# Performance work log

Hardware: AMD Instinct MI355X
Metric: run time of the kernel (lower is better)

The kernel has to match this reference:

```python
import jax, jax.numpy as jnp
import numpy as np

B, T, C, H, W = 2, 20, 128, 128, 128
D_MODEL = 256
N_HEAD = 16
D_K = 4
MLP_OUT = 128
PE_T = 1000.0
EPS = 1e-5


def setup_inputs() -> dict:
    key = jax.random.key(0)
    ks = jax.random.split(key, 16)
    x = jax.random.normal(ks[0], (B, T, C, H, W), jnp.float32)
    batch_positions = jnp.sort(
        jax.random.randint(ks[1], (B, T), 0, 365).astype(jnp.int32), axis=1)
    qk_std = float(np.sqrt(2.0 / D_K))
    return {
        "x": x,
        "batch_positions": batch_positions,
        # GroupNorm(n_head, in_channels)
        "in_norm_w": jnp.ones((C,), jnp.float32),
        "in_norm_b": jnp.zeros((C,), jnp.float32),
        # Conv1d(in_channels, d_model, 1) -> weight (d_model, in_channels)
        "inconv_w": jax.random.normal(ks[2], (D_MODEL, C), jnp.float32) / np.sqrt(C),
        "inconv_b": jax.random.normal(ks[3], (D_MODEL,), jnp.float32) * 0.01,
        # learnable query (n_head, d_k), std sqrt(2/d_k)
        "Q": jax.random.normal(ks[4], (N_HEAD, D_K), jnp.float32) * qk_std,
        # fc1_k: Linear(d_model, n_head*d_k)
        "k_w": jax.random.normal(ks[5], (N_HEAD * D_K, D_MODEL), jnp.float32) * qk_std,
        "k_b": jax.random.normal(ks[6], (N_HEAD * D_K,), jnp.float32) * 0.01,
        # MLP: Linear(256, 128) + LayerNorm(128)
        "mlp_w": jax.random.normal(ks[7], (MLP_OUT, D_MODEL), jnp.float32) / np.sqrt(D_MODEL),
        "mlp_b": jax.random.normal(ks[8], (MLP_OUT,), jnp.float32) * 0.01,
        "ln_w": jnp.ones((MLP_OUT,), jnp.float32),
        "ln_b": jnp.zeros((MLP_OUT,), jnp.float32),
        # out GroupNorm(n_head, mlp[-1])
        "out_norm_w": jnp.ones((MLP_OUT,), jnp.float32),
        "out_norm_b": jnp.zeros((MLP_OUT,), jnp.float32),
    }


def _ltae_forward(x, batch_positions, in_norm_w, in_norm_b, inconv_w, inconv_b,
                  Q, k_w, k_b, mlp_w, mlp_b, ln_w, ln_b, out_norm_w, out_norm_b):
    b, t, c, h, w = x.shape
    n_head, d_k = Q.shape
    n = b * h * w
    # (B,T,C,H,W) -> (N, T, C), N = B*H*W ordered (b, h, w)
    out = jnp.transpose(x, (0, 3, 4, 1, 2)).reshape(n, t, c)

    # in_norm: GroupNorm(groups=n_head) over (group-channels, T) per sample
    cg = c // n_head
    xg = out.reshape(n, t, n_head, cg)
    mu = xg.mean(axis=(1, 3), keepdims=True)
    var = xg.var(axis=(1, 3), keepdims=True)
    out = ((xg - mu) / jnp.sqrt(var + EPS)).reshape(n, t, c) * in_norm_w + in_norm_b

    # inconv: 1x1 Conv1d == per-timestep linear (C -> d_model)
    out = out @ inconv_w.T + inconv_b  # (N, T, d_model)
    d_model = out.shape[-1]

    # sinusoidal positional encoding (d_model//n_head dims, repeated n_head times)
    d_pe = d_model // n_head
    i = jnp.arange(d_pe)
    denom = PE_T ** (2.0 * (i // 2).astype(out.dtype) / d_pe)
    bp = batch_positions.astype(out.dtype)  # (B, T)
    tab = bp[:, :, None] / denom            # (B, T, d_pe)
    pe = jnp.where(i % 2 == 0, jnp.sin(tab), jnp.cos(tab))
    pe = jnp.tile(pe, (1, 1, n_head))        # (B, T, d_model)
    out = (out.reshape(b, h, w, t, d_model) + pe[:, None, None]).reshape(n, t, d_model)

    # multi-head attention pooling with one learnable query per head
    k = (out @ k_w.T + k_b).reshape(n, t, n_head, d_k)
    scores = jnp.einsum('nthd,hd->nht', k, Q) / jnp.sqrt(jnp.asarray(d_k, out.dtype))
    attn = jax.nn.softmax(scores, axis=-1)             # (N, H, T)
    vh = out.reshape(n, t, n_head, d_model // n_head)  # head h = channel slice
    pooled = jnp.einsum('nht,nthe->nhe', attn, vh).reshape(n, d_model)

    # MLP: Linear -> LayerNorm -> GELU (exact)
    h1 = pooled @ mlp_w.T + mlp_b
    mu = h1.mean(-1, keepdims=True)
    var = h1.var(-1, keepdims=True)
    h1 = (h1 - mu) / jnp.sqrt(var + EPS) * ln_w + ln_b
    h1 = jax.nn.gelu(h1, approximate=False)

    # out_norm: GroupNorm(n_head) on (N, mlp_out) -> stats over each group's channels
    co = h1.shape[-1]
    xg = h1.reshape(n, n_head, co // n_head)
    mu = xg.mean(-1, keepdims=True)
    var = xg.var(-1, keepdims=True)
    h1 = ((xg - mu) / jnp.sqrt(var + EPS)).reshape(n, co) * out_norm_w + out_norm_b

    return h1.reshape(b, h, w, co).transpose(0, 3, 1, 2)  # (B, mlp_out, H, W)


def reference(x, batch_positions, in_norm_w, in_norm_b, inconv_w, inconv_b,
              Q, k_w, k_b, mlp_w, mlp_b, ln_w, ln_b, out_norm_w, out_norm_b):
    return _ltae_forward(x, batch_positions, in_norm_w, in_norm_b, inconv_w,
                         inconv_b, Q, k_w, k_b, mlp_w, mlp_b, ln_w, ln_b,
                         out_norm_w, out_norm_b)
```

## Files before the change

### kernel.cpp

```cpp
#include <hip/hip_runtime.h>
#include <hip/hip_fp16.h>

typedef _Float16 h2  __attribute__((ext_vector_type(2)));
typedef _Float16 v8h __attribute__((ext_vector_type(8)));
typedef float    f4  __attribute__((ext_vector_type(4)));
typedef uint4 u128;

#define T_    20
#define C_    128
#define HW_   16384
#define NH_   16
#define TILE_ 16
#define EPSV  1e-5f

#define OFF_SW   0
#define OFF_SC   4096
#define OFF_WC   8192
#define OFF_MW   73728
#define OFF_PBT  139264
#define OFF_MB2  141312

__device__ __forceinline__ float fdot2f(h2 a, h2 b, float c) {
#if __has_builtin(__builtin_amdgcn_fdot2)
  return __builtin_amdgcn_fdot2(a, b, c, false);
#else
  return c + (float)a[0]*(float)b[0] + (float)a[1]*(float)b[1];
#endif
}

__device__ __forceinline__ v8h zero8() {
  v8h r;
  #pragma unroll
  for (int i = 0; i < 8; ++i) r[i] = (_Float16)0.f;
  return r;
}

__global__ void __launch_bounds__(256) ltae_prep(
    const int* __restrict__ bp, const float* __restrict__ gw, const float* __restrict__ gb,
    const float* __restrict__ icw, const float* __restrict__ icb,
    const float* __restrict__ Qm, const float* __restrict__ kw, const float* __restrict__ kb,
    const float* __restrict__ mw, const float* __restrict__ mb,
    unsigned char* __restrict__ ws)
{
  const int tid = threadIdx.x;
  const int blk = blockIdx.x;
  _Float16* SWh = (_Float16*)(ws + OFF_SW);
  float*    SC  = (float*)(ws + OFF_SC);
  _Float16* WCf = (_Float16*)(ws + OFF_WC);
  _Float16* MWf = (_Float16*)(ws + OFF_MW);
  _Float16* PBT = (_Float16*)(ws + OFF_PBT);
  float*    MB2 = (float*)(ws + OFF_MB2);

  __shared__ float qwl[16*256];
  __shared__ float bcl[256];
  __shared__ float pet[2*20*16];
  __shared__ float qbl[16];
  __shared__ float qwsl[16*16];

  if (blk < 4) {
    for (int o = tid; o < 512; o += 256) {
      int h = 4*blk + (o >> 7), c = o & 127;
      float q0 = Qm[h*4+0], q1 = Qm[h*4+1], q2 = Qm[h*4+2], q3 = Qm[h*4+3];
      const float* k0 = kw + (4*h+0)*256;
      const float* k1 = kw + (4*h+1)*256;
      const float* k2 = kw + (4*h+2)*256;
      const float* k3 = kw + (4*h+3)*256;
      float acc = 0.f;
      for (int d = 0; d < 256; ++d) {
        float qwd = k0[d]*q0 + k1[d]*q1 + k2[d]*q2 + k3[d]*q3;
        acc = fmaf(icw[d*128 + c], qwd, acc);
      }
      SWh[h*128 + c] = (_Float16)(acc * gw[c]);
    }
  } else if (blk < 6) {
    int base = (blk - 4) * 16384;
    for (int o = tid; o < 16384; o += 256) {
      int idx = base + o;
      WCf[idx] = (_Float16)(icw[idx] * gw[idx & 127]);
    }
  } else if (blk < 8) {
    int base = (blk - 6) * 16384;
    for (int o = tid; o < 16384; o += 256)
      MWf[base + o] = (_Float16)mw[base + o];
  } else if (blk == 8) {
    if (tid < 256) {
      float a = icb[tid];
      for (int c2 = 0; c2 < 128; ++c2) a = fmaf(gb[c2], icw[tid*128 + c2], a);
      bcl[tid] = a;
    }
    __syncthreads();
    if (tid < 128) {
      float a = mb[tid];
      for (int d = 0; d < 256; ++d) a = fmaf(bcl[d], mw[tid*256 + d], a);
      MB2[tid] = a;
    }
  } else {
    for (int o = tid; o < 4096; o += 256) {
      int h = o >> 8, d = o & 255;
      qwl[o] = kw[(4*h+0)*256+d]*Qm[h*4+0] + kw[(4*h+1)*256+d]*Qm[h*4+1]
             + kw[(4*h+2)*256+d]*Qm[h*4+2] + kw[(4*h+3)*256+d]*Qm[h*4+3];
    }
    if (tid < 256) {
      float a = icb[tid];
      for (int c2 = 0; c2 < 128; ++c2) a = fmaf(gb[c2], icw[tid*128 + c2], a);
      bcl[tid] = a;
    }
    for (int o = tid; o < 640; o += 256) {
      int bb = o / 320, rem = o % 320;
      int t = rem >> 4, e = rem & 15;
      float pos = (float)bp[bb*T_ + t];
      float den = powf(1000.f, (float)(2*(e>>1)) / 16.f);
      float v = pos / den;
      pet[o] = (e & 1) ? cosf(v) : sinf(v);
    }
    __syncthreads();
    if (tid < 16) {
      qbl[tid] = kb[tid*4+0]*Qm[tid*4+0] + kb[tid*4+1]*Qm[tid*4+1]
               + kb[tid*4+2]*Qm[tid*4+2] + kb[tid*4+3]*Qm[tid*4+3];
    }
    if (tid < 256) {
      int h = tid >> 4, e = tid & 15;
      float a = 0.f;
      for (int m2 = 0; m2 < 16; ++m2) a += qwl[h*256 + m2*16 + e];
      qwsl[tid] = a;
    }
    __syncthreads();
    for (int o = tid; o < 640; o += 256) {
      int bb = o / 320, rem = o % 320;
      int t = rem >> 4, h = rem & 15;
      float a = qbl[h];
      for (int d = 0; d < 256; ++d) a = fmaf(bcl[d], qwl[h*256 + d], a);
      for (int e = 0; e < 16; ++e) a = fmaf(pet[(bb*T_ + t)*16 + e], qwsl[h*16 + e], a);
      SC[(bb*T_ + t)*NH_ + h] = 0.5f * a;
    }
    for (int o = tid; o < 1024; o += 256) {
      int bb = o >> 9, e = (o >> 5) & 15, tp = o & 31;
      PBT[o] = (tp < T_) ? (_Float16)pet[(bb*T_ + tp)*16 + e] : (_Float16)0.f;
    }
  }
}

__global__ void __launch_bounds__(256, 2) ltae_main(
    const float* __restrict__ x, const unsigned char* __restrict__ ws,
    float* __restrict__ out,
    const float* __restrict__ lnw, const float* __restrict__ lnb,
    const float* __restrict__ onw, const float* __restrict__ onb)
{
  __shared__ __align__(16) unsigned char lds[81920];
  const int tid = threadIdx.x;
  const int s = tid >> 4, q = tid & 15;
  const int lane = tid & 63;

  int bid = (int)blockIdx.x;
  int L = (bid & 7) * 256 + (bid >> 3);
  const int n0 = L * TILE_;
  const int b  = n0 >> 14;
  const int r0 = n0 & 16383;

  #define XS(row, chunk) ((unsigned char*)lds + (row)*256 + ((((chunk) ^ ((row)&7))) << 4))

  float gsum = 0.f, gsq = 0.f;
  {
    const float* p = x + (size_t)b*(T_*C_*HW_) + (size_t)(q*8)*HW_ + r0 + s;
    for (int t = 0; t < T_; ++t) {
      float v[8];
      #pragma unroll
      for (int i = 0; i < 8; ++i) v[i] = p[(size_t)i*HW_];
      p += (size_t)C_*HW_;
      #pragma unroll
      for (int i = 0; i < 8; ++i) { gsum += v[i]; gsq = fmaf(v[i], v[i], gsq); }
      u128 pk; h2* ph = (h2*)&pk;
      #pragma unroll
      for (int i = 0; i < 4; ++i) { h2 t2; t2[0] = (_Float16)v[2*i]; t2[1] = (_Float16)v[2*i+1]; ph[i] = t2; }
      *(u128*)XS(t*16 + s, q) = pk;
    }
  }
  float mug[16], invg[16];
  {
    float mu  = gsum * (1.f/160.f);
    float var = fmaf(-mu, mu, gsq * (1.f/160.f));
    float inv = rsqrtf(var + EPSV);
    int lb = lane & 48;
    #pragma unroll
    for (int g = 0; g < 16; ++g) {
      mug[g]  = __shfl(mu,  lb + g, 64);
      invg[g] = __shfl(inv, lb + g, 64);
    }
  }
  __syncthreads();

  float a_[T_];
  {
    h2 sw[64];
    {
      const u128* sp = (const u128*)(ws + OFF_SW) + q*16;
      #pragma unroll
      for (int i = 0; i < 16; ++i) ((u128*)sw)[i] = sp[i];
    }
    float K0 = 0.f;
    #pragma unroll
    for (int g = 0; g < 16; ++g) {
      float ss = 0.f;
      #pragma unroll
      for (int k = 0; k < 4; ++k) ss += (float)sw[g*4+k][0] + (float)sw[g*4+k][1];
      K0 = fmaf(invg[g]*mug[g], ss, K0);
    }
    const float* SCp = (const float*)(ws + OFF_SC) + (b*T_)*NH_ + q;
    #pragma unroll
    for (int t = 0; t < T_; ++t) {
      int row = t*16 + s;
      float accE = 0.f, accO = 0.f;
      #pragma unroll
      for (int g = 0; g < 16; g += 2) {
        u128 u0 = *(const u128*)XS(row, g);
        u128 u1 = *(const u128*)XS(row, g+1);
        h2* x0 = (h2*)&u0; h2* x1 = (h2*)&u1;
        float s0 = 0.f, s1 = 0.f;
        #pragma unroll
        for (int k = 0; k < 4; ++k) {
          s0 = fdot2f(x0[k], sw[g*4+k],     s0);
          s1 = fdot2f(x1[k], sw[(g+1)*4+k], s1);
        }
        accE = fmaf(invg[g],   s0, accE);
        accO = fmaf(invg[g+1], s1, accO);
      }
      a_[t] = 0.5f*((accE + accO) - K0) + SCp[t*NH_];
    }
  }
  h2 ah[T_];
  {
    float m = a_[0];
    #pragma unroll
    for (int t = 1; t < T_; ++t) m = fmaxf(m, a_[t]);
    float Z = 0.f;
    #pragma unroll
    for (int t = 0; t < T_; ++t) { a_[t] = __expf(a_[t] - m); Z += a_[t]; }
    float rZ = 1.f / Z;
    #pragma unroll
    for (int t = 0; t < T_; ++t) {
      a_[t] *= rZ;
      _Float16 af = (_Float16)a_[t];
      h2 t2; t2[0] = af; t2[1] = af; ah[t] = t2;
    }
  }

  #pragma unroll 1
  for (int g = 0; g < 16; ++g) {
    h2 accA[4], accB[4];
    #pragma unroll
    for (int k = 0; k < 4; ++k) { accA[k][0]=(_Float16)0.f; accA[k][1]=(_Float16)0.f;
                                  accB[k][0]=(_Float16)0.f; accB[k][1]=(_Float16)0.f; }
    #pragma unroll
    for (int t = 0; t < T_; t += 2) {
      u128 u0 = *(const u128*)XS(t*16 + s, g);
      u128 u1 = *(const u128*)XS((t+1)*16 + s, g);
      h2* x0 = (h2*)&u0; h2* x1 = (h2*)&u1;
      #pragma unroll
      for (int k = 0; k < 4; ++k) {
        accA[k] = ah[t]  * x0[k] + accA[k];
        accB[k] = ah[t+1]* x1[k] + accB[k];
      }
    }
    __syncthreads();
    u128 pk; h2* ph = (h2*)&pk;
    #pragma unroll
    for (int k = 0; k < 4; ++k) {
      float lo = (float)accA[k][0] + (float)accB[k][0];
      float hi = (float)accA[k][1] + (float)accB[k][1];
      lo = invg[g]*(lo - mug[g]);
      hi = invg[g]*(hi - mug[g]);
      h2 t2; t2[0] = (_Float16)lo; t2[1] = (_Float16)hi; ph[k] = t2;
    }
    *(u128*)XS(q*16 + s, g) = pk;
  }

  {
    unsigned char* atl = lds + 65536 + (q*16 + s)*48;
    u128 pk0, pk1, pk2;
    h2* p0 = (h2*)&pk0; h2* p1 = (h2*)&pk1; h2* p2 = (h2*)&pk2;
    #pragma unroll
    for (int k = 0; k < 4; ++k) { h2 t2; t2[0]=(_Float16)a_[2*k];   t2[1]=(_Float16)a_[2*k+1]; p0[k]=t2; }
    #pragma unroll
    for (int k = 0; k < 4; ++k) { h2 t2; t2[0]=(_Float16)a_[8+2*k]; t2[1]=(_Float16)a_[9+2*k]; p1[k]=t2; }
    #pragma unroll
    for (int k = 0; k < 4; ++k) {
      h2 t2;
      t2[0] = (k<2) ? (_Float16)a_[16+2*k] : (_Float16)0.f;
      t2[1] = (k<2) ? (_Float16)a_[17+2*k] : (_Float16)0.f;
      p2[k]=t2;
    }
    *(u128*)(atl) = pk0; *(u128*)(atl+16) = pk1; *(u128*)(atl+32) = pk2;
  }
  __syncthreads();

  const int wid = tid >> 6;
  const int lr = lane & 15, lk = lane >> 4;
  f4 pacc[4];
  {
    const _Float16* WC  = (const _Float16*)(ws + OFF_WC);
    const _Float16* PBT = (const _Float16*)(ws + OFF_PBT);
    #pragma unroll
    for (int hh = 0; hh < 4; ++hh) {
      int h = wid*4 + hh;
      f4 acc = {0.f,0.f,0.f,0.f};
      #pragma unroll
      for (int ks = 0; ks < 4; ++ks) {
        v8h A = *(const v8h*)XS(h*16 + lr, ks*4 + lk);
        v8h B = *(const v8h*)(WC + (16*h + lr)*128 + ks*32 + lk*8);
        acc = __builtin_amdgcn_mfma_f32_16x16x32_f16(A, B, acc, 0, 0, 0);
      }
      {
        v8h A = zero8();
        if (lk < 3) A = *(const v8h*)(lds + 65536 + (h*16 + lr)*48 + lk*16);
        v8h B = *(const v8h*)(PBT + (b*16 + lr)*32 + lk*8);
        acc = __builtin_amdgcn_mfma_f32_16x16x32_f16(A, B, acc, 0, 0, 0);
      }
      pacc[hh] = acc;
    }
  }
  __syncthreads();
  #pragma unroll
  for (int hh = 0; hh < 4; ++hh) {
    int d = 16*(wid*4 + hh) + lr;
    #pragma unroll
    for (int r = 0; r < 4; ++r) {
      int sp = 4*lk + r;
      *(_Float16*)(lds + ((sp*512 + d*2) ^ ((sp&7)<<4))) = (_Float16)pacc[hh][r];
    }
  }
  __syncthreads();

  f4 m0 = {0.f,0.f,0.f,0.f}, m1 = {0.f,0.f,0.f,0.f};
  {
    const _Float16* MW = (const _Float16*)(ws + OFF_MW);
    #pragma unroll
    for (int ks = 0; ks < 8; ++ks) {
      int d0 = ks*32 + lk*8;
      v8h A  = *(const v8h*)(lds + ((lr*512 + d0*2) ^ ((lr&7)<<4)));
      v8h B0 = *(const v8h*)(MW + (32*wid + lr)*256 + d0);
      v8h B1 = *(const v8h*)(MW + (32*wid + 16 + lr)*256 + d0);
      m0 = __builtin_amdgcn_mfma_f32_16x16x32_f16(A, B0, m0, 0,0,0);
      m1 = __builtin_amdgcn_mfma_f32_16x16x32_f16(A, B1, m1, 0,0,0);
    }
  }
  {
    const float* MB2 = (const float*)(ws + OFF_MB2);
    int j0 = 32*wid + lr, j1 = 32*wid + 16 + lr;
    float b0 = MB2[j0], b1 = MB2[j1];
    #pragma unroll
    for (int r = 0; r < 4; ++r) {
      int sp = 4*lk + r;
      *(float*)(lds + 8192 + ((sp*512 + j0*4) ^ ((sp&7)<<4))) = m0[r] + b0;
      *(float*)(lds + 8192 + ((sp*512 + j1*4) ^ ((sp&7)<<4))) = m1[r] + b1;
    }
  }
  __syncthreads();

  {
    float4 A0 = *(const float4*)(lds + 8192 + (((s*512 + q*32)      ) ^ ((s&7)<<4)));
    float4 A1 = *(const float4*)(lds + 8192 + (((s*512 + q*32 + 16) ) ^ ((s&7)<<4)));
    float h1v[8] = {A0.x,A0.y,A0.z,A0.w,A1.x,A1.y,A1.z,A1.w};
    float sum = 0.f, sq = 0.f;
    #pragma unroll
    for (int i = 0; i < 8; ++i) { sum += h1v[i]; sq = fmaf(h1v[i], h1v[i], sq); }
    #pragma unroll
    for (int d = 1; d < 16; d <<= 1) { sum += __shfl_xor(sum, d, 64); sq += __shfl_xor(sq, d, 64); }
    float mu1 = sum * (1.f/128.f);
    float vr1 = fmaf(-mu1, mu1, sq * (1.f/128.f));
    float is1 = rsqrtf(vr1 + EPSV);
    float4 lwa = *(const float4*)(lnw + 8*q), lwb = *(const float4*)(lnw + 8*q + 4);
    float4 lba = *(const float4*)(lnb + 8*q), lbb = *(const float4*)(lnb + 8*q + 4);
    float lw[8] = {lwa.x,lwa.y,lwa.z,lwa.w,lwb.x,lwb.y,lwb.z,lwb.w};
    float lb2[8] = {lba.x,lba.y,lba.z,lba.w,lbb.x,lbb.y,lbb.z,lbb.w};
    float yv[8]; float s2 = 0.f, q2 = 0.f;
    #pragma unroll
    for (int i = 0; i < 8; ++i) {
      float g_ = (h1v[i]-mu1)*is1*lw[i] + lb2[i];
      float y  = 0.5f*g_*(1.f + erff(g_*0.70710678118654752f));
      yv[i] = y; s2 += y; q2 = fmaf(y, y, q2);
    }
    s2 *= 0.125f;
    float v2 = fmaf(-s2, s2, q2*0.125f);
    float iv2 = rsqrtf(v2 + EPSV);
    float4 owa = *(const float4*)(onw + 8*q), owb = *(const float4*)(onw + 8*q + 4);
    float4 oba = *(const float4*)(onb + 8*q), obb = *(const float4*)(onb + 8*q + 4);
    float ow[8] = {owa.x,owa.y,owa.z,owa.w,owb.x,owb.y,owb.z,owb.w};
    float ob[8] = {oba.x,oba.y,oba.z,oba.w,obb.x,obb.y,obb.z,obb.w};
    float* op = out + (size_t)(b*128 + 8*q)*HW_ + r0 + s;
    #pragma unroll
    for (int i = 0; i < 8; ++i)
      op[(size_t)i*HW_] = (yv[i]-s2)*iv2*ow[i] + ob[i];
  }
  #undef XS
}

extern "C" void kernel_launch(void* const* d_in, const int* in_sizes, int n_in,
                              void* d_out, int out_size, void* d_ws, size_t ws_size,
                              hipStream_t stream) {
  const float* x   = (const float*)d_in[0];
  const int*   bp  = (const int*)d_in[1];
  const float* gw  = (const float*)d_in[2];
  const float* gb  = (const float*)d_in[3];
  const float* icw = (const float*)d_in[4];
  const float* icb = (const float*)d_in[5];
  const float* Qm  = (const float*)d_in[6];
  const float* kw  = (const float*)d_in[7];
  const float* kb  = (const float*)d_in[8];
  const float* mw  = (const float*)d_in[9];
  const float* mb  = (const float*)d_in[10];
  const float* lnw = (const float*)d_in[11];
  const float* lnb = (const float*)d_in[12];
  const float* onw = (const float*)d_in[13];
  const float* onb = (const float*)d_in[14];
  unsigned char* ws = (unsigned char*)d_ws;

  hipLaunchKernelGGL(ltae_prep, dim3(10), dim3(256), 0, stream,
                     bp, gw, gb, icw, icb, Qm, kw, kb, mw, mb, ws);
  hipLaunchKernelGGL(ltae_main, dim3(2048), dim3(256), 0, stream,
                     x, ws, (float*)d_out, lnw, lnb, onw, onb);
}
```

Baseline: 657.4 us.

## Restructure main kernel for 512 threads with MFMA attention scores and vectorized I/O

The main kernel moves to 512-thread blocks. Input loads become float4 reads across pixels, GroupNorm statistics are reduced through LDS, and the input is normalized before it is stored. Attention scores are computed with MFMA instead of fdot2 loops, and the weighted pooling is remapped across threads using shuffles. The output is transposed through LDS so stores are float4. The prep kernel splits the SW computation over 16 blocks. Together these aim to cut global memory transactions, raise occupancy and shorten the prep kernel, at the cost of more barriers, more shuffle traffic and higher register pressure.

After: 603.3 us. 8.2% less time.

```diff
diff --git a/kernel.cpp b/kernel.cpp
--- a/kernel.cpp
+++ b/kernel.cpp
@@ -20,20 +20,14 @@
 #define OFF_PBT  139264
 #define OFF_MB2  141312
 
-__device__ __forceinline__ float fdot2f(h2 a, h2 b, float c) {
-#if __has_builtin(__builtin_amdgcn_fdot2)
-  return __builtin_amdgcn_fdot2(a, b, c, false);
-#else
-  return c + (float)a[0]*(float)b[0] + (float)a[1]*(float)b[1];
-#endif
-}
-
 __device__ __forceinline__ v8h zero8() {
   v8h r;
   #pragma unroll
   for (int i = 0; i < 8; ++i) r[i] = (_Float16)0.f;
   return r;
 }
+__device__ __forceinline__ int h2i(h2 v) { union { h2 h; int i; } u; u.h = v; return u.i; }
+__device__ __forceinline__ h2  ih2(int v) { union { h2 h; int i; } u; u.i = v; return u.h; }
 
 __global__ void __launch_bounds__(256) ltae_prep(
     const int* __restrict__ bp, const float* __restrict__ gw, const float* __restrict__ gb,
@@ -56,33 +50,36 @@
   __shared__ float pet[2*20*16];
   __shared__ float qbl[16];
   __shared__ float qwsl[16*16];
-
-  if (blk < 4) {
-    for (int o = tid; o < 512; o += 256) {
-      int h = 4*blk + (o >> 7), c = o & 127;
-      float q0 = Qm[h*4+0], q1 = Qm[h*4+1], q2 = Qm[h*4+2], q3 = Qm[h*4+3];
-      const float* k0 = kw + (4*h+0)*256;
-      const float* k1 = kw + (4*h+1)*256;
-      const float* k2 = kw + (4*h+2)*256;
-      const float* k3 = kw + (4*h+3)*256;
-      float acc = 0.f;
-      for (int d = 0; d < 256; ++d) {
-        float qwd = k0[d]*q0 + k1[d]*q1 + k2[d]*q2 + k3[d]*q3;
-        acc = fmaf(icw[d*128 + c], qwd, acc);
-      }
-      SWh[h*128 + c] = (_Float16)(acc * gw[c]);
-    }
-  } else if (blk < 6) {
-    int base = (blk - 4) * 16384;
+  __shared__ float red[256];
+
+  if (blk < 16) {
+    int h = blk, dh = tid >> 7;
+    float q0 = Qm[h*4+0], q1 = Qm[h*4+1], q2 = Qm[h*4+2], q3 = Qm[h*4+3];
+    const float* k0 = kw + (4*h+0)*256;
+    const float* k1 = kw + (4*h+1)*256;
+    const float* k2 = kw + (4*h+2)*256;
+    const float* k3 = kw + (4*h+3)*256;
+    int c = tid & 127;
+    float acc = 0.f;
+    for (int d = 0; d < 128; ++d) {
+      int dg = dh*128 + d;
+      float qwd = k0[dg]*q0 + k1[dg]*q1 + k2[dg]*q2 + k3[dg]*q3;
+      acc = fmaf(icw[dg*128 + c], qwd, acc);
+    }
+    red[tid] = acc;
+    __syncthreads();
+    if (tid < 128) SWh[h*128 + tid] = (_Float16)((red[tid] + red[tid+128]) * gw[tid] * 0.5f);
+  } else if (blk < 18) {
+    int base = (blk - 16) * 16384;
     for (int o = tid; o < 16384; o += 256) {
       int idx = base + o;
       WCf[idx] = (_Float16)(icw[idx] * gw[idx & 127]);
     }
-  } else if (blk < 8) {
-    int base = (blk - 6) * 16384;
+  } else if (blk < 20) {
+    int base = (blk - 18) * 16384;
     for (int o = tid; o < 16384; o += 256)
       MWf[base + o] = (_Float16)mw[base + o];
-  } else if (blk == 8) {
+  } else if (blk == 20) {
     if (tid < 256) {
       float a = icb[tid];
       for (int c2 = 0; c2 < 128; ++c2) a = fmaf(gb[c2], icw[tid*128 + c2], a);
@@ -140,16 +137,17 @@
   }
 }
 
-__global__ void __launch_bounds__(256, 2) ltae_main(
+__global__ void __launch_bounds__(512, 4) ltae_main(
     const float* __restrict__ x, const unsigned char* __restrict__ ws,
     float* __restrict__ out,
     const float* __restrict__ lnw, const float* __restrict__ lnb,
     const float* __restrict__ onw, const float* __restrict__ onb)
 {
   __shared__ __align__(16) unsigned char lds[81920];
-  const int tid = threadIdx.x;
-  const int s = tid >> 4, q = tid & 15;
+  const int tid  = threadIdx.x;
   const int lane = tid & 63;
+  const int w    = tid >> 6;
+  const int m16  = lane & 15, kg = lane >> 4;
 
   int bid = (int)blockIdx.x;
   int L = (bid & 7) * 256 + (bid >> 3);
@@ -157,241 +155,325 @@
   const int b  = n0 >> 14;
   const int r0 = n0 & 16383;
 
-  #define XS(row, chunk) ((unsigned char*)lds + (row)*256 + ((((chunk) ^ ((row)&7))) << 4))
-
-  float gsum = 0.f, gsq = 0.f;
-  {
-    const float* p = x + (size_t)b*(T_*C_*HW_) + (size_t)(q*8)*HW_ + r0 + s;
-    for (int t = 0; t < T_; ++t) {
-      float v[8];
-      #pragma unroll
-      for (int i = 0; i < 8; ++i) v[i] = p[(size_t)i*HW_];
-      p += (size_t)C_*HW_;
-      #pragma unroll
-      for (int i = 0; i < 8; ++i) { gsum += v[i]; gsq = fmaf(v[i], v[i], gsq); }
-      u128 pk; h2* ph = (h2*)&pk;
-      #pragma unroll
-      for (int i = 0; i < 4; ++i) { h2 t2; t2[0] = (_Float16)v[2*i]; t2[1] = (_Float16)v[2*i+1]; ph[i] = t2; }
-      *(u128*)XS(t*16 + s, q) = pk;
-    }
-  }
-  float mug[16], invg[16];
-  {
-    float mu  = gsum * (1.f/160.f);
-    float var = fmaf(-mu, mu, gsq * (1.f/160.f));
-    float inv = rsqrtf(var + EPSV);
-    int lb = lane & 48;
-    #pragma unroll
-    for (int g = 0; g < 16; ++g) {
-      mug[g]  = __shfl(mu,  lb + g, 64);
-      invg[g] = __shfl(inv, lb + g, 64);
-    }
-  }
-  __syncthreads();
-
-  float a_[T_];
-  {
-    h2 sw[64];
-    {
-      const u128* sp = (const u128*)(ws + OFF_SW) + q*16;
-      #pragma unroll
-      for (int i = 0; i < 16; ++i) ((u128*)sw)[i] = sp[i];
-    }
-    float K0 = 0.f;
-    #pragma unroll
-    for (int g = 0; g < 16; ++g) {
-      float ss = 0.f;
-      #pragma unroll
-      for (int k = 0; k < 4; ++k) ss += (float)sw[g*4+k][0] + (float)sw[g*4+k][1];
-      K0 = fmaf(invg[g]*mug[g], ss, K0);
-    }
-    const float* SCp = (const float*)(ws + OFF_SC) + (b*T_)*NH_ + q;
-    #pragma unroll
-    for (int t = 0; t < T_; ++t) {
-      int row = t*16 + s;
-      float accE = 0.f, accO = 0.f;
-      #pragma unroll
-      for (int g = 0; g < 16; g += 2) {
-        u128 u0 = *(const u128*)XS(row, g);
-        u128 u1 = *(const u128*)XS(row, g+1);
-        h2* x0 = (h2*)&u0; h2* x1 = (h2*)&u1;
-        float s0 = 0.f, s1 = 0.f;
+#define XS(row, chunk) ((unsigned char*)lds + (row)*256 + \
+    ((((chunk) ^ (((row) ^ ((row) >> 4)) & 15))) << 4))
+#define PL(s, byteo) ((unsigned char*)lds + (s)*512 + \
+    (((((byteo) >> 4) ^ (((s)*2) & 31))) << 4) + ((byteo) & 15))
+#define HL(s, byteo) ((unsigned char*)lds + 8192 + (s)*512 + \
+    (((((byteo) >> 4) ^ (((s)*2) & 31))) << 4) + ((byteo) & 15))
+
+  {
+    const int sub = tid & 3, g = (tid >> 2) & 15, w8 = w;
+    uint2 hp[20];
+    float ps0=0,ps1=0,ps2=0,ps3=0, pq0=0,pq1=0,pq2=0,pq3=0;
+    const float* xb = x + (size_t)b*(T_*C_*HW_) + r0 + 4*sub;
+    #pragma unroll
+    for (int k = 0; k < 20; ++k) {
+      int j = w8 + 8*k;
+      int t = j >> 3, cg = j & 7, c = g*8 + cg;
+      float4 v = *(const float4*)(xb + (size_t)(t*C_ + c) * HW_);
+      ps0 += v.x; pq0 = fmaf(v.x, v.x, pq0);
+      ps1 += v.y; pq1 = fmaf(v.y, v.y, pq1);
+      ps2 += v.z; pq2 = fmaf(v.z, v.z, pq2);
+      ps3 += v.w; pq3 = fmaf(v.w, v.w, pq3);
+      h2 lo; lo[0] = (_Float16)v.x; lo[1] = (_Float16)v.y;
+      h2 hi; hi[0] = (_Float16)v.z; hi[1] = (_Float16)v.w;
+      hp[k] = make_uint2((unsigned)h2i(lo), (unsigned)h2i(hi));
+    }
+    unsigned char* scr = (unsigned char*)lds + 65536;
+    float psum[4] = {ps0,ps1,ps2,ps3}, psq[4] = {pq0,pq1,pq2,pq3};
+    #pragma unroll
+    for (int i = 0; i < 4; ++i) {
+      int s = 4*sub + i;
+      int word = w8*512 + g*32 + (((s + g) & 15) << 1);
+      *(float2*)(scr + word*4) = make_float2(psum[i], psq[i]);
+    }
+    __syncthreads();
+    float mu[4], inv[4];
+    #pragma unroll
+    for (int i = 0; i < 4; ++i) {
+      int s = 4*sub + i;
+      float su = 0.f, sq = 0.f;
+      #pragma unroll
+      for (int ww = 0; ww < 8; ++ww) {
+        float2 p = *(const float2*)(scr + (ww*512 + g*32 + (((s + g) & 15) << 1))*4);
+        su += p.x; sq += p.y;
+      }
+      float m_ = su * (1.f/160.f);
+      mu[i]  = m_;
+      inv[i] = rsqrtf(fmaf(-m_, m_, sq * (1.f/160.f)) + EPSV);
+    }
+#define P1WRITE(k) { \
+      int j = w8 + 8*(k); \
+      int t = j >> 3, cg = j & 7; \
+      h2 lo = ih2((int)hp[k].x), hi = ih2((int)hp[k].y); \
+      float f0 = ((float)lo[0] - mu[0]) * inv[0]; \
+      float f1 = ((float)lo[1] - mu[1]) * inv[1]; \
+      float f2 = ((float)hi[0] - mu[2]) * inv[2]; \
+      float f3 = ((float)hi[1] - mu[3]) * inv[3]; \
+      *(_Float16*)(XS(t*16 + 4*sub + 0, g) + cg*2) = (_Float16)f0; \
+      *(_Float16*)(XS(t*16 + 4*sub + 1, g) + cg*2) = (_Float16)f1; \
+      *(_Float16*)(XS(t*16 + 4*sub + 2, g) + cg*2) = (_Float16)f2; \
+      *(_Float16*)(XS(t*16 + 4*sub + 3, g) + cg*2) = (_Float16)f3; }
+    #pragma unroll
+    for (int k = 0; k < 16; ++k) P1WRITE(k)
+    __syncthreads();
+    #pragma unroll
+    for (int k = 16; k < 20; ++k) P1WRITE(k)
+#undef P1WRITE
+  }
+  __syncthreads();
+
+  float attA[2][4], attB[2][4];
+  {
+    v8h Bsw[4];
+    const _Float16* SWp = (const _Float16*)(ws + OFF_SW) + m16*128 + kg*8;
+    #pragma unroll
+    for (int ks = 0; ks < 4; ++ks) Bsw[ks] = *(const v8h*)(SWp + ks*32);
+    const float* SCb = (const float*)(ws + OFF_SC) + b*T_*NH_;
+    #pragma unroll
+    for (int si = 0; si < 2; ++si) {
+      int s = 2*w + si;
+      f4 a0 = {0.f,0.f,0.f,0.f}, a1 = {0.f,0.f,0.f,0.f};
+      #pragma unroll
+      for (int ks = 0; ks < 4; ++ks) {
+        v8h A = *(const v8h*)XS(m16*16 + s, ks*4 + kg);
+        a0 = __builtin_amdgcn_mfma_f32_16x16x32_f16(A, Bsw[ks], a0, 0, 0, 0);
+        v8h At = zero8();
+        if (m16 < 4) At = *(const v8h*)XS((16 + m16)*16 + s, ks*4 + kg);
+        a1 = __builtin_amdgcn_mfma_f32_16x16x32_f16(At, Bsw[ks], a1, 0, 0, 0);
+      }
+      float aa[4], ab[4] = {0.f,0.f,0.f,0.f};
+      #pragma unroll
+      for (int r = 0; r < 4; ++r) aa[r] = a0[r] + SCb[(4*kg + r)*NH_ + m16];
+      if (kg == 0) {
         #pragma unroll
-        for (int k = 0; k < 4; ++k) {
-          s0 = fdot2f(x0[k], sw[g*4+k],     s0);
-          s1 = fdot2f(x1[k], sw[(g+1)*4+k], s1);
-        }
-        accE = fmaf(invg[g],   s0, accE);
-        accO = fmaf(invg[g+1], s1, accO);
-      }
-      a_[t] = 0.5f*((accE + accO) - K0) + SCp[t*NH_];
-    }
-  }
-  h2 ah[T_];
-  {
-    float m = a_[0];
-    #pragma unroll
-    for (int t = 1; t < T_; ++t) m = fmaxf(m, a_[t]);
-    float Z = 0.f;
-    #pragma unroll
-    for (int t = 0; t < T_; ++t) { a_[t] = __expf(a_[t] - m); Z += a_[t]; }
-    float rZ = 1.f / Z;
-    #pragma unroll
-    for (int t = 0; t < T_; ++t) {
-      a_[t] *= rZ;
-      _Float16 af = (_Float16)a_[t];
-      h2 t2; t2[0] = af; t2[1] = af; ah[t] = t2;
-    }
-  }
-
-  #pragma unroll 1
-  for (int g = 0; g < 16; ++g) {
-    h2 accA[4], accB[4];
-    #pragma unroll
-    for (int k = 0; k < 4; ++k) { accA[k][0]=(_Float16)0.f; accA[k][1]=(_Float16)0.f;
-                                  accB[k][0]=(_Float16)0.f; accB[k][1]=(_Float16)0.f; }
-    #pragma unroll
-    for (int t = 0; t < T_; t += 2) {
-      u128 u0 = *(const u128*)XS(t*16 + s, g);
-      u128 u1 = *(const u128*)XS((t+1)*16 + s, g);
-      h2* x0 = (h2*)&u0; h2* x1 = (h2*)&u1;
-      #pragma unroll
-      for (int k = 0; k < 4; ++k) {
-        accA[k] = ah[t]  * x0[k] + accA[k];
-        accB[k] = ah[t+1]* x1[k] + accB[k];
-      }
-    }
-    __syncthreads();
-    u128 pk; h2* ph = (h2*)&pk;
-    #pragma unroll
-    for (int k = 0; k < 4; ++k) {
-      float lo = (float)accA[k][0] + (float)accB[k][0];
-      float hi = (float)accA[k][1] + (float)accB[k][1];
-      lo = invg[g]*(lo - mug[g]);
-      hi = invg[g]*(hi - mug[g]);
-      h2 t2; t2[0] = (_Float16)lo; t2[1] = (_Float16)hi; ph[k] = t2;
-    }
-    *(u128*)XS(q*16 + s, g) = pk;
-  }
-
-  {
-    unsigned char* atl = lds + 65536 + (q*16 + s)*48;
-    u128 pk0, pk1, pk2;
-    h2* p0 = (h2*)&pk0; h2* p1 = (h2*)&pk1; h2* p2 = (h2*)&pk2;
-    #pragma unroll
-    for (int k = 0; k < 4; ++k) { h2 t2; t2[0]=(_Float16)a_[2*k];   t2[1]=(_Float16)a_[2*k+1]; p0[k]=t2; }
-    #pragma unroll
-    for (int k = 0; k < 4; ++k) { h2 t2; t2[0]=(_Float16)a_[8+2*k]; t2[1]=(_Float16)a_[9+2*k]; p1[k]=t2; }
-    #pragma unroll
-    for (int k = 0; k < 4; ++k) {
-      h2 t2;
-      t2[0] = (k<2) ? (_Float16)a_[16+2*k] : (_Float16)0.f;
-      t2[1] = (k<2) ? (_Float16)a_[17+2*k] : (_Float16)0.f;
-      p2[k]=t2;
-    }
-    *(u128*)(atl) = pk0; *(u128*)(atl+16) = pk1; *(u128*)(atl+32) = pk2;
-  }
-  __syncthreads();
-
-  const int wid = tid >> 6;
-  const int lr = lane & 15, lk = lane >> 4;
-  f4 pacc[4];
+        for (int r = 0; r < 4; ++r) ab[r] = a1[r] + SCb[(16 + r)*NH_ + m16];
+      }
+      float mx = fmaxf(fmaxf(aa[0], aa[1]), fmaxf(aa[2], aa[3]));
+      if (kg == 0) mx = fmaxf(mx, fmaxf(fmaxf(ab[0], ab[1]), fmaxf(ab[2], ab[3])));
+      mx = fmaxf(mx, __shfl_xor(mx, 16, 64));
+      mx = fmaxf(mx, __shfl_xor(mx, 32, 64));
+      float Z = 0.f;
+      #pragma unroll
+      for (int r = 0; r < 4; ++r) { aa[r] = __expf(aa[r] - mx); Z += aa[r]; }
+      if (kg == 0) {
+        #pragma unroll
+        for (int r = 0; r < 4; ++r) { ab[r] = __expf(ab[r] - mx); Z += ab[r]; }
+      }
+      Z += __shfl_xor(Z, 16, 64);
+      Z += __shfl_xor(Z, 32, 64);
+      float rZ = 1.f / Z;
+      #pragma unroll
+      for (int r = 0; r < 4; ++r) {
+        attA[si][r] = aa[r] * rZ;
+        attB[si][r] = (kg == 0) ? ab[r] * rZ : 0.f;
+      }
+    }
+  }
+  int qi0,qi1,qi2,qi3, qb0,qb1,qb2,qb3;
+  {
+    h2 p;
+    p[0]=(_Float16)attA[0][0]; p[1]=(_Float16)attA[1][0]; qi0=h2i(p);
+    p[0]=(_Float16)attA[0][1]; p[1]=(_Float16)attA[1][1]; qi1=h2i(p);
+    p[0]=(_Float16)attA[0][2]; p[1]=(_Float16)attA[1][2]; qi2=h2i(p);
+    p[0]=(_Float16)attA[0][3]; p[1]=(_Float16)attA[1][3]; qi3=h2i(p);
+    p[0]=(_Float16)attB[0][0]; p[1]=(_Float16)attB[1][0]; qb0=h2i(p);
+    p[0]=(_Float16)attB[0][1]; p[1]=(_Float16)attB[1][1]; qb1=h2i(p);
+    p[0]=(_Float16)attB[0][2]; p[1]=(_Float16)attB[1][2]; qb2=h2i(p);
+    p[0]=(_Float16)attB[0][3]; p[1]=(_Float16)attB[1][3]; qb3=h2i(p);
+  }
+
+  const int sP = tid >> 5;
+  const int ll = lane & 31, hq = ll >> 3, cp = ll & 7;
+  const int hiHalf = (lane >> 5) & 1;
+  h2 acc0[4][8], acc1[4][8];
+  #pragma unroll
+  for (int i = 0; i < 4; ++i)
+    #pragma unroll
+    for (int c2 = 0; c2 < 8; ++c2) {
+      acc0[i][c2][0] = (_Float16)0.f; acc0[i][c2][1] = (_Float16)0.f;
+      acc1[i][c2][0] = (_Float16)0.f; acc1[i][c2][1] = (_Float16)0.f;
+    }
+  #pragma unroll
+  for (int t = 0; t < T_; t += 2) {
+    u128 u0 = *(const u128*)XS(t*16 + sP, 2*cp);
+    u128 u1 = *(const u128*)XS(t*16 + sP, 2*cp + 1);
+    u128 w0 = *(const u128*)XS((t+1)*16 + sP, 2*cp);
+    u128 w1 = *(const u128*)XS((t+1)*16 + sP, 2*cp + 1);
+    const h2* e0 = (const h2*)&u0; const h2* e1 = (const h2*)&u1;
+    const h2* f0 = (const h2*)&w0; const h2* f1 = (const h2*)&w1;
+    int qselE = (t < 16) ? (((t & 3) == 0) ? qi0 : qi2) : (((t & 3) == 0) ? qb0 : qb2);
+    int qselO = (t < 16) ? (((t & 3) == 0) ? qi1 : qi3) : (((t & 3) == 0) ? qb1 : qb3);
+    #pragma unroll
+    for (int i = 0; i < 4; ++i) {
+      int h = 4*hq + i;
+      int src = (t < 16) ? (h + ((t >> 2) << 4)) : h;
+      h2 pvE = ih2(__shfl(qselE, src, 64));
+      h2 pvO = ih2(__shfl(qselO, src, 64));
+      _Float16 aE = hiHalf ? pvE[1] : pvE[0];
+      _Float16 aO = hiHalf ? pvO[1] : pvO[0];
+      h2 aE2; aE2[0] = aE; aE2[1] = aE;
+      h2 aO2; aO2[0] = aO; aO2[1] = aO;
+      #pragma unroll
+      for (int c2 = 0; c2 < 4; ++c2) {
+        acc0[i][c2]     = aE2 * e0[c2] + acc0[i][c2];
+        acc0[i][4 + c2] = aE2 * e1[c2] + acc0[i][4 + c2];
+        acc1[i][c2]     = aO2 * f0[c2] + acc1[i][c2];
+        acc1[i][4 + c2] = aO2 * f1[c2] + acc1[i][4 + c2];
+      }
+    }
+  }
+  __syncthreads();
+  #pragma unroll
+  for (int i = 0; i < 4; ++i) {
+    int h = 4*hq + i;
+    u128 o0, o1;
+    h2* p0 = (h2*)&o0; h2* p1 = (h2*)&o1;
+    #pragma unroll
+    for (int c2 = 0; c2 < 8; ++c2) {
+      float lo = (float)acc0[i][c2][0] + (float)acc1[i][c2][0];
+      float hi = (float)acc0[i][c2][1] + (float)acc1[i][c2][1];
+      h2 t2; t2[0] = (_Float16)lo; t2[1] = (_Float16)hi;
+      if (c2 < 4) p0[c2] = t2; else p1[c2 - 4] = t2;
+    }
+    *(u128*)XS(h*16 + sP, 2*cp)     = o0;
+    *(u128*)XS(h*16 + sP, 2*cp + 1) = o1;
+  }
+  {
+    unsigned char* atl = (unsigned char*)lds + 65536;
+    #pragma unroll
+    for (int si = 0; si < 2; ++si) {
+      int s = 2*w + si;
+      #pragma unroll
+      for (int r = 0; r < 4; ++r)
+        *(_Float16*)(atl + (m16*16 + s)*64 + (4*kg + r)*2) = (_Float16)attA[si][r];
+    }
+    if (kg == 0) {
+      #pragma unroll
+      for (int si = 0; si < 2; ++si) {
+        int s = 2*w + si;
+        #pragma unroll
+        for (int r = 0; r < 4; ++r)
+          *(_Float16*)(atl + (m16*16 + s)*64 + (16 + r)*2) = (_Float16)attB[si][r];
+      }
+    }
+    if (tid < 256) {
+      unsigned char* zp = atl + tid*64 + 40;
+      *(uint2*)(zp)      = make_uint2(0u, 0u);
+      *(uint2*)(zp + 8)  = make_uint2(0u, 0u);
+      *(uint2*)(zp + 16) = make_uint2(0u, 0u);
+    }
+  }
+  __syncthreads();
+
+  f4 pacc[2];
   {
     const _Float16* WC  = (const _Float16*)(ws + OFF_WC);
     const _Float16* PBT = (const _Float16*)(ws + OFF_PBT);
-    #pragma unroll
-    for (int hh = 0; hh < 4; ++hh) {
-      int h = wid*4 + hh;
-      f4 acc = {0.f,0.f,0.f,0.f};
+    const unsigned char* atl = (const unsigned char*)lds + 65536;
+    #pragma unroll
+    for (int hh = 0; hh < 2; ++hh) {
+      int hs = 2*w + hh;
+      f4 a2 = {0.f,0.f,0.f,0.f};
       #pragma unroll
       for (int ks = 0; ks < 4; ++ks) {
-        v8h A = *(const v8h*)XS(h*16 + lr, ks*4 + lk);
-        v8h B = *(const v8h*)(WC + (16*h + lr)*128 + ks*32 + lk*8);
-        acc = __builtin_amdgcn_mfma_f32_16x16x32_f16(A, B, acc, 0, 0, 0);
-      }
-      {
-        v8h A = zero8();
-        if (lk < 3) A = *(const v8h*)(lds + 65536 + (h*16 + lr)*48 + lk*16);
-        v8h B = *(const v8h*)(PBT + (b*16 + lr)*32 + lk*8);
-        acc = __builtin_amdgcn_mfma_f32_16x16x32_f16(A, B, acc, 0, 0, 0);
-      }
-      pacc[hh] = acc;
+        v8h A = *(const v8h*)XS(hs*16 + m16, ks*4 + kg);
+        v8h B = *(const v8h*)(WC + (16*hs + m16)*128 + ks*32 + kg*8);
+        a2 = __builtin_amdgcn_mfma_f32_16x16x32_f16(A, B, a2, 0, 0, 0);
+      }
+      v8h A2 = *(const v8h*)(atl + (hs*16 + m16)*64 + kg*16);
+      v8h B2 = *(const v8h*)(PBT + (b*16 + m16)*32 + kg*8);
+      a2 = __builtin_amdgcn_mfma_f32_16x16x32_f16(A2, B2, a2, 0, 0, 0);
+      pacc[hh] = a2;
     }
   }
   __syncthreads();
   #pragma unroll
-  for (int hh = 0; hh < 4; ++hh) {
-    int d = 16*(wid*4 + hh) + lr;
+  for (int hh = 0; hh < 2; ++hh) {
+    int hs = 2*w + hh;
+    int d = 16*hs + m16;
     #pragma unroll
     for (int r = 0; r < 4; ++r) {
-      int sp = 4*lk + r;
-      *(_Float16*)(lds + ((sp*512 + d*2) ^ ((sp&7)<<4))) = (_Float16)pacc[hh][r];
-    }
-  }
-  __syncthreads();
-
-  f4 m0 = {0.f,0.f,0.f,0.f}, m1 = {0.f,0.f,0.f,0.f};
-  {
+      int other = __shfl_xor(__float_as_int(pacc[hh][r]), 1, 64);
+      if ((m16 & 1) == 0) {
+        h2 pk2; pk2[0] = (_Float16)pacc[hh][r]; pk2[1] = (_Float16)__int_as_float(other);
+        *(int*)PL(4*kg + r, d*2) = h2i(pk2);
+      }
+    }
+  }
+  __syncthreads();
+
+  {
+    f4 macc = {0.f,0.f,0.f,0.f};
     const _Float16* MW = (const _Float16*)(ws + OFF_MW);
     #pragma unroll
     for (int ks = 0; ks < 8; ++ks) {
-      int d0 = ks*32 + lk*8;
-      v8h A  = *(const v8h*)(lds + ((lr*512 + d0*2) ^ ((lr&7)<<4)));
-      v8h B0 = *(const v8h*)(MW + (32*wid + lr)*256 + d0);
-      v8h B1 = *(const v8h*)(MW + (32*wid + 16 + lr)*256 + d0);
-      m0 = __builtin_amdgcn_mfma_f32_16x16x32_f16(A, B0, m0, 0,0,0);
-      m1 = __builtin_amdgcn_mfma_f32_16x16x32_f16(A, B1, m1, 0,0,0);
-    }
-  }
-  {
+      v8h A = *(const v8h*)PL(m16, ks*64 + kg*16);
+      v8h B = *(const v8h*)(MW + (16*w + m16)*256 + ks*32 + kg*8);
+      macc = __builtin_amdgcn_mfma_f32_16x16x32_f16(A, B, macc, 0, 0, 0);
+    }
     const float* MB2 = (const float*)(ws + OFF_MB2);
-    int j0 = 32*wid + lr, j1 = 32*wid + 16 + lr;
-    float b0 = MB2[j0], b1 = MB2[j1];
-    #pragma unroll
-    for (int r = 0; r < 4; ++r) {
-      int sp = 4*lk + r;
-      *(float*)(lds + 8192 + ((sp*512 + j0*4) ^ ((sp&7)<<4))) = m0[r] + b0;
-      *(float*)(lds + 8192 + ((sp*512 + j1*4) ^ ((sp&7)<<4))) = m1[r] + b1;
-    }
-  }
-  __syncthreads();
-
-  {
-    float4 A0 = *(const float4*)(lds + 8192 + (((s*512 + q*32)      ) ^ ((s&7)<<4)));
-    float4 A1 = *(const float4*)(lds + 8192 + (((s*512 + q*32 + 16) ) ^ ((s&7)<<4)));
-    float h1v[8] = {A0.x,A0.y,A0.z,A0.w,A1.x,A1.y,A1.z,A1.w};
+    int j = 16*w + m16;
+    float bj = MB2[j];
+    #pragma unroll
+    for (int r = 0; r < 4; ++r)
+      *(float*)HL(4*kg + r, j*4) = macc[r] + bj;
+  }
+  __syncthreads();
+
+  {
+    const int sF = tid >> 5, rF = tid & 31;
+    float4 A0 = *(const float4*)HL(sF, rF*16);
+    float h1v[4] = {A0.x, A0.y, A0.z, A0.w};
     float sum = 0.f, sq = 0.f;
     #pragma unroll
-    for (int i = 0; i < 8; ++i) { sum += h1v[i]; sq = fmaf(h1v[i], h1v[i], sq); }
-    #pragma unroll
-    for (int d = 1; d < 16; d <<= 1) { sum += __shfl_xor(sum, d, 64); sq += __shfl_xor(sq, d, 64); }
+    for (int i = 0; i < 4; ++i) { sum += h1v[i]; sq = fmaf(h1v[i], h1v[i], sq); }
+    #pragma unroll
+    for (int d = 1; d < 32; d <<= 1) { sum += __shfl_xor(sum, d, 64); sq += __shfl_xor(sq, d, 64); }
     float mu1 = sum * (1.f/128.f);
     float vr1 = fmaf(-mu1, mu1, sq * (1.f/128.f));
     float is1 = rsqrtf(vr1 + EPSV);
-    float4 lwa = *(const float4*)(lnw + 8*q), lwb = *(const float4*)(lnw + 8*q + 4);
-    float4 lba = *(const float4*)(lnb + 8*q), lbb = *(const float4*)(lnb + 8*q + 4);
-    float lw[8] = {lwa.x,lwa.y,lwa.z,lwa.w,lwb.x,lwb.y,lwb.z,lwb.w};
-    float lb2[8] = {lba.x,lba.y,lba.z,lba.w,lbb.x,lbb.y,lbb.z,lbb.w};
-    float yv[8]; float s2 = 0.f, q2 = 0.f;
-    #pragma unroll
-    for (int i = 0; i < 8; ++i) {
-      float g_ = (h1v[i]-mu1)*is1*lw[i] + lb2[i];
+    float4 lw4 = *(const float4*)(lnw + 4*rF);
+    float4 lb4 = *(const float4*)(lnb + 4*rF);
+    float lw[4] = {lw4.x, lw4.y, lw4.z, lw4.w};
+    float lb2[4] = {lb4.x, lb4.y, lb4.z, lb4.w};
+    float yv[4]; float ys = 0.f, yq = 0.f;
+    #pragma unroll
+    for (int i = 0; i < 4; ++i) {
+      float g_ = (h1v[i] - mu1)*is1*lw[i] + lb2[i];
       float y  = 0.5f*g_*(1.f + erff(g_*0.70710678118654752f));
-      yv[i] = y; s2 += y; q2 = fmaf(y, y, q2);
-    }
-    s2 *= 0.125f;
-    float v2 = fmaf(-s2, s2, q2*0.125f);
+      yv[i] = y; ys += y; yq = fmaf(y, y, yq);
+    }
+    ys += __shfl_xor(ys, 1, 64);
+    yq += __shfl_xor(yq, 1, 64);
+    float m2  = ys * 0.125f;
+    float v2  = fmaf(-m2, m2, yq * 0.125f);
     float iv2 = rsqrtf(v2 + EPSV);
-    float4 owa = *(const float4*)(onw + 8*q), owb = *(const float4*)(onw + 8*q + 4);
-    float4 oba = *(const float4*)(onb + 8*q), obb = *(const float4*)(onb + 8*q + 4);
-    float ow[8] = {owa.x,owa.y,owa.z,owa.w,owb.x,owb.y,owb.z,owb.w};
-    float ob[8] = {oba.x,oba.y,oba.z,oba.w,obb.x,obb.y,obb.z,obb.w};
-    float* op = out + (size_t)(b*128 + 8*q)*HW_ + r0 + s;
-    #pragma unroll
-    for (int i = 0; i < 8; ++i)
-      op[(size_t)i*HW_] = (yv[i]-s2)*iv2*ow[i] + ob[i];
-  }
-  #undef XS
+    float4 ow4 = *(const float4*)(onw + 4*rF);
+    float4 ob4 = *(const float4*)(onb + 4*rF);
+    float ow[4] = {ow4.x, ow4.y, ow4.z, ow4.w};
+    float ob[4] = {ob4.x, ob4.y, ob4.z, ob4.w};
+    float4 yo;
+    yo.x = (yv[0]-m2)*iv2*ow[0] + ob[0];
+    yo.y = (yv[1]-m2)*iv2*ow[1] + ob[1];
+    yo.z = (yv[2]-m2)*iv2*ow[2] + ob[2];
+    yo.w = (yv[3]-m2)*iv2*ow[3] + ob[3];
+    *(float4*)HL(sF, rF*16) = yo;
+  }
+  __syncthreads();
+  {
+    int jT = tid >> 2, sq4 = tid & 3;
+    float4 o;
+    o.x = *(const float*)HL(4*sq4 + 0, jT*4);
+    o.y = *(const float*)HL(4*sq4 + 1, jT*4);
+    o.z = *(const float*)HL(4*sq4 + 2, jT*4);
+    o.w = *(const float*)HL(4*sq4 + 3, jT*4);
+    *(float4*)(out + (size_t)(b*128 + jT)*HW_ + r0 + 4*sq4) = o;
+  }
+#undef XS
+#undef PL
+#undef HL
 }
 
 extern "C" void kernel_launch(void* const* d_in, const int* in_sizes, int n_in,
@@ -414,8 +496,8 @@
   const float* onb = (const float*)d_in[14];
   unsigned char* ws = (unsigned char*)d_ws;
 
-  hipLaunchKernelGGL(ltae_prep, dim3(10), dim3(256), 0, stream,
+  hipLaunchKernelGGL(ltae_prep, dim3(22), dim3(256), 0, stream,
                      bp, gw, gb, icw, icb, Qm, kw, kb, mw, mb, ws);
-  hipLaunchKernelGGL(ltae_main, dim3(2048), dim3(256), 0, stream,
+  hipLaunchKernelGGL(ltae_main, dim3(2048), dim3(512), 0, stream,
                      x, ws, (float*)d_out, lnw, lnb, onw, onb);
 }
```
